# Performance work log

Measured on AMD Instinct MI355X. Metric: run time of the kernel, lower is better.

The kernel has to match this reference:

```python
import math
import jax, jax.numpy as jnp
import numpy as np

K_KDE = 50
K_RIPS = 16
SCALE = 30.0
DESTNUM = 10
THRESHOLD = 1.0  # hardcoded in topograd_loss
N, D = 8192, 64


def _knn(x, k):
    """Brute-force k-NN with squared L2 distances (faiss IndexFlatL2 semantics,
    self included as nearest neighbour). Returns (sq_dists[N,k], idxs[N,k]),
    neighbours sorted by increasing distance."""
    sq = jnp.sum(x * x, axis=1)
    d = sq[:, None] + sq[None, :] - 2.0 * (x @ x.T)  # [N,N]
    neg, idx = jax.lax.top_k(-d, k)
    return -neg, idx


def _cluster(density, rips_idxs, threshold):
    """Union-find re-implementation of the numba `cluster` routine.
    Iterates points from high density (index N-1) to low; each point joins the
    entry of its highest-index upward neighbour; other upward neighbours'
    entries are merged if their persistence is below threshold, and every
    cross-entry comparison emits a persistence pair (entry_idx, ref_idx).
    Returns the raw pers_pairs array (without the [-1,-1] sentinel rows)."""
    n = density.shape[0]
    parent = np.arange(n)
    name = np.arange(n)  # name[root] = entry id (a point index)

    def find(i):
        root = i
        while parent[root] != root:
            root = parent[root]
        while parent[i] != root:  # path compression
            parent[i], i = root, parent[i]
        return root

    pairs = []
    for i in range(n - 2, -1, -1):
        nbr = rips_idxs[i]
        us = nbr[nbr > i]  # upward (denser, already-processed) neighbours
        if us.size == 0:
            continue  # point i forms its own singleton entry
        e_up = name[find(int(us.max()))]
        parent[find(i)] = find(e_up)  # append i to entry e_up
        for j in us:
            ei = name[find(int(j))]
            if ei != e_up:
                pairs.append((ei, i))
                if density[ei] - density[i] < threshold:
                    parent[find(ei)] = find(e_up)  # merge entry ei into e_up
    return np.asarray(pairs, dtype=np.int64).reshape(-1, 2)


def _pd_pairs(pairs, n):
    """For each unique entry id in pairs[:,0], keep (entry_id, max ref idx)."""
    maxref = np.full(n, -1, dtype=np.int64)
    np.maximum.at(maxref, pairs[:, 0], pairs[:, 1])
    uniq = np.unique(pairs[:, 0])
    return np.stack([uniq, maxref[uniq]], axis=1)


def setup_inputs() -> dict:
    key = jax.random.key(0)
    x = jax.random.normal(key, (N, D), dtype=jnp.float32)
    return {"x": x}


def reference(x):
    # --- KNN kernel density estimate (differentiable) ---
    vals, _ = _knn(x, K_KDE)
    res = jnp.sum(jnp.exp(-vals / SCALE), axis=1) / (K_KDE * SCALE)
    dens = res / jnp.max(res)
    # --- sort by ascending density ---
    sorted_idxs = jnp.argsort(dens)
    dens_s = dens[sorted_idxs]
    x_s = x[sorted_idxs]
    # --- delta-Rips graph on sorted points ---
    _, rips_idxs = _knn(x_s, K_RIPS)
    # --- persistence clustering (non-differentiable, host) ---
    pairs = _cluster(np.asarray(dens_s), np.asarray(rips_idxs), THRESHOLD)
    pd = jnp.asarray(_pd_pairs(pairs, x.shape[0]))  # [P,2] int64
    # --- topological loss ---
    oripd = dens_s[pd]  # [P,2] (birth, death) densities
    sidx = jnp.argsort(oripd[:, 0] - oripd[:, 1])  # ascending persistence
    changepairs = pd[sidx[:-DESTNUM]]
    nochangepairs = pd[sidx[-DESTNUM:-1]]
    dest = jax.lax.stop_gradient(oripd[sidx[-1]])  # torch.as_tensor detaches
    pd11 = dens_s[changepairs]
    weakdist = jnp.sum(pd11[:, 0] - pd11[:, 1]) / math.sqrt(2.0)
    strongdist = jnp.sum(jnp.linalg.norm(dens_s[nochangepairs] - dest, axis=1))
    return weakdist + strongdist
```

## Files before the change

### kernel.cpp

```cpp
#include <hip/hip_runtime.h>
#include <stdint.h>

#define NN 8192
#define DD 64

using bf16x8 = __attribute__((ext_vector_type(8))) short;
using f32x4  = __attribute__((ext_vector_type(4))) float;

__device__ __forceinline__ unsigned short f2bf(float f){
  unsigned u = __float_as_uint(f);
  return (unsigned short)((u + 0x7FFFu + ((u >> 16) & 1u)) >> 16);
}

__device__ __forceinline__ unsigned long long shfl64_xor(unsigned long long v, int off){
  return (((unsigned long long)(unsigned)__shfl_xor((int)(v >> 32), off)) << 32)
       | (unsigned long long)(unsigned)__shfl_xor((int)(v & 0xFFFFFFFFu), off);
}

__global__ __launch_bounds__(256) void k_pre(const float* __restrict__ x, float* __restrict__ xT,
                                             float* __restrict__ sq, int do_tr,
                                             uint4* __restrict__ xfrag, int do_frag){
  __shared__ float tile[64*65];
  const int tid = threadIdx.x;
  const int b = blockIdx.x;
  for (int k = 0; k < 4; ++k){
    const int idx4 = tid + k*256;
    const float4 v = ((const float4*)(x + (size_t)b*4096))[idx4];
    const int row = idx4 >> 4, d0 = (idx4 & 15) * 4;
    tile[row*65 + d0 + 0] = v.x;
    tile[row*65 + d0 + 1] = v.y;
    tile[row*65 + d0 + 2] = v.z;
    tile[row*65 + d0 + 3] = v.w;
  }
  __syncthreads();
  if (do_tr){
    const int jj = tid & 15;
    const int dq = tid >> 4;
    for (int k = 0; k < 4; ++k){
      const int d = dq + 16*k;
      float4 o;
      o.x = tile[(jj*4+0)*65 + d];
      o.y = tile[(jj*4+1)*65 + d];
      o.z = tile[(jj*4+2)*65 + d];
      o.w = tile[(jj*4+3)*65 + d];
      ((float4*)xT)[(size_t)d*2048 + b*16 + jj] = o;
    }
  }
  if (do_frag){
    for (int ch = tid; ch < 512; ch += 256){
      const int c  = ch & 15;
      const int q  = (ch >> 4) & 3;
      const int m  = (ch >> 6) & 1;
      const int gl = ch >> 7;
      const float* sp = tile + (gl*16 + c)*65 + m*32 + q*8;
      unsigned short h[8];
#pragma unroll
      for (int i2 = 0; i2 < 8; ++i2) h[i2] = f2bf(sp[i2]);
      uint4 o;
      o.x = (unsigned)h[0] | ((unsigned)h[1] << 16);
      o.y = (unsigned)h[2] | ((unsigned)h[3] << 16);
      o.z = (unsigned)h[4] | ((unsigned)h[5] << 16);
      o.w = (unsigned)h[6] | ((unsigned)h[7] << 16);
      xfrag[(size_t)b*512 + ch] = o;
    }
  }
  if (tid < 64){
    float acc = 0.f;
    const float* rp = tile + tid*65;
    for (int d = 0; d < 64; ++d) acc = fmaf(rp[d], rp[d], acc);
    sq[b*64 + tid] = acc;
  }
}

template<bool XT>
__device__ __forceinline__ void dists_1024(const float* __restrict__ x, const float* __restrict__ xT,
                                           const float* __restrict__ xi, int jbase, int tid,
                                           float acc[8][4]){
#pragma unroll
  for (int r = 0; r < 8; ++r)
#pragma unroll
    for (int q = 0; q < 4; ++q) acc[r][q] = 0.f;
  const int j0 = jbase + tid*4;
  for (int dq = 0; dq < 16; ++dq){
    float4 vj[4];
    if (XT){
#pragma unroll
      for (int s = 0; s < 4; ++s)
        vj[s] = ((const float4*)xT)[(size_t)(dq*4+s)*2048 + (j0 >> 2)];
    } else {
#pragma unroll
      for (int s = 0; s < 4; ++s){
        const int d = dq*4 + s;
        vj[s].x = x[(size_t)(j0+0)*64 + d];
        vj[s].y = x[(size_t)(j0+1)*64 + d];
        vj[s].z = x[(size_t)(j0+2)*64 + d];
        vj[s].w = x[(size_t)(j0+3)*64 + d];
      }
    }
#pragma unroll
    for (int r = 0; r < 8; ++r){
      const float4 wv = ((const float4*)(xi + r*64))[dq];
      acc[r][0] = fmaf(vj[0].x, wv.x, acc[r][0]);
      acc[r][1] = fmaf(vj[0].y, wv.x, acc[r][1]);
      acc[r][2] = fmaf(vj[0].z, wv.x, acc[r][2]);
      acc[r][3] = fmaf(vj[0].w, wv.x, acc[r][3]);
      acc[r][0] = fmaf(vj[1].x, wv.y, acc[r][0]);
      acc[r][1] = fmaf(vj[1].y, wv.y, acc[r][1]);
      acc[r][2] = fmaf(vj[1].z, wv.y, acc[r][2]);
      acc[r][3] = fmaf(vj[1].w, wv.y, acc[r][3]);
      acc[r][0] = fmaf(vj[2].x, wv.z, acc[r][0]);
      acc[r][1] = fmaf(vj[2].y, wv.z, acc[r][1]);
      acc[r][2] = fmaf(vj[2].z, wv.z, acc[r][2]);
      acc[r][3] = fmaf(vj[2].w, wv.z, acc[r][3]);
      acc[r][0] = fmaf(vj[3].x, wv.w, acc[r][0]);
      acc[r][1] = fmaf(vj[3].y, wv.w, acc[r][1]);
      acc[r][2] = fmaf(vj[3].z, wv.w, acc[r][2]);
      acc[r][3] = fmaf(vj[3].w, wv.w, acc[r][3]);
    }
  }
}

template<bool XT>
__global__ __launch_bounds__(256) void k_samp(const float* __restrict__ x, const float* __restrict__ xT,
                                              const float* __restrict__ sq, float* __restrict__ tub){
  __shared__ __align__(16) float xi[8*64];
  __shared__ float sqi_s[8];
  __shared__ __align__(16) float samp[8*1024];
  const int tid = threadIdx.x;
  const int i0 = blockIdx.x * 8;
  for (int t = tid; t < 8*64; t += 256) xi[t] = x[(size_t)i0*64 + t];
  if (tid < 8) sqi_s[tid] = sq[i0+tid];
  __syncthreads();
  float sqir[8];
#pragma unroll
  for (int r = 0; r < 8; ++r) sqir[r] = sqi_s[r];

  const int w0 = (blockIdx.x * 1024) & 8191;
  float acc[8][4];
  dists_1024<XT>(x, xT, xi, w0, tid, acc);
  float sqj[4];
#pragma unroll
  for (int q = 0; q < 4; ++q) sqj[q] = sq[w0 + tid*4 + q];
#pragma unroll
  for (int r = 0; r < 8; ++r)
#pragma unroll
    for (int q = 0; q < 4; ++q)
      samp[r*1024 + tid*4 + q] = (sqir[r] + sqj[q]) - 2.f*acc[r][q];
  __syncthreads();
  const int wv = tid >> 6, lane = tid & 63;
  for (int rr = 0; rr < 2; ++rr){
    const int r = wv + rr*4;
    float v[16];
#pragma unroll
    for (int k2 = 0; k2 < 16; ++k2) v[k2] = samp[r*1024 + lane + 64*k2];
    unsigned lo = 0u, hi = 0x7F800001u;
    while (hi - lo > 1u){
      const unsigned mid = (lo + hi) >> 1;
      const float pf = __uint_as_float(mid);
      int c = 0;
#pragma unroll
      for (int k2 = 0; k2 < 16; ++k2) c += (v[k2] < pf) ? 1 : 0;
#pragma unroll
      for (int off = 32; off; off >>= 1) c += __shfl_xor(c, off);
      if (c >= 32) hi = mid; else lo = mid;
    }
    if (lane == 0) tub[i0 + r] = __uint_as_float(hi);
  }
}

__global__ __launch_bounds__(256) void k_filt(const float* __restrict__ x, const float* __restrict__ sq,
                                              const float* __restrict__ tub,
                                              const uint4* __restrict__ xfrag,
                                              unsigned char* __restrict__ nib){
  const int tid = threadIdx.x;
  const int l   = tid & 63;
  const int w   = tid >> 6;
  const int qh  = l >> 4;
  const int c16 = l & 15;
  const int i0  = blockIdx.x * 8;

  bf16x8 a0, a1;
#pragma unroll
  for (int i2 = 0; i2 < 8; ++i2){ a0[i2] = 0; a1[i2] = 0; }
  if (c16 < 8){
    const float* ap = x + (size_t)(i0 + c16)*64 + qh*8;
#pragma unroll
    for (int i2 = 0; i2 < 8; ++i2){
      a0[i2] = (short)f2bf(ap[i2]);
      a1[i2] = (short)f2bf(ap[i2 + 32]);
    }
  }
  float thr3[4], rs[4];
#pragma unroll
  for (int rg = 0; rg < 4; ++rg){
    int row = qh*4 + rg; row = (row < 8) ? row : 0;
    thr3[rg] = (tub[i0 + row] - sq[i0 + row]) + 0.002f;
    rs[rg]   = 0.017f * sqrtf(sq[i0 + row]);
  }

  const bf16x8* bfp = (const bf16x8*)xfrag + (size_t)w*128 + l;
  const float*  sqp = sq + w*16 + c16;
  unsigned char* nb = nib + (size_t)blockIdx.x*8192 + w*16 + c16;

  bf16x8 A0 = bfp[0],   A1 = bfp[64];     float SA = sqp[0];
  bf16x8 B0 = bfp[512], B1 = bfp[512+64]; float SB = sqp[64];
  for (int it = 0; it < 128; it += 2){
    const int n2 = (it+2 < 128) ? it+2 : 126;
    const int n3 = (it+3 < 128) ? it+3 : 127;
    bf16x8 N0 = bfp[(size_t)n2*512], N1 = bfp[(size_t)n2*512 + 64];
    bf16x8 M0 = bfp[(size_t)n3*512], M1 = bfp[(size_t)n3*512 + 64];
    const float SN = sqp[n2*64], SM = sqp[n3*64];
    {
      f32x4 acc = {0.f, 0.f, 0.f, 0.f};
      acc = __builtin_amdgcn_mfma_f32_16x16x32_bf16(a0, A0, acc, 0, 0, 0);
      acc = __builtin_amdgcn_mfma_f32_16x16x32_bf16(a1, A1, acc, 0, 0, 0);
      const float sr = sqrtf(SA);
      unsigned m4 = 0u;
      m4 |= (fmaf(-rs[0], sr, fmaf(-2.f, acc[0], SA)) < thr3[0]) ? 1u : 0u;
      m4 |= (fmaf(-rs[1], sr, fmaf(-2.f, acc[1], SA)) < thr3[1]) ? 2u : 0u;
      m4 |= (fmaf(-rs[2], sr, fmaf(-2.f, acc[2], SA)) < thr3[2]) ? 4u : 0u;
      m4 |= (fmaf(-rs[3], sr, fmaf(-2.f, acc[3], SA)) < thr3[3]) ? 8u : 0u;
      const unsigned pm = (unsigned)__shfl((int)m4, (l + 16) & 63);
      if (l < 16) nb[it*64] = (unsigned char)(m4 | (pm << 4));
    }
    {
      f32x4 acc = {0.f, 0.f, 0.f, 0.f};
      acc = __builtin_amdgcn_mfma_f32_16x16x32_bf16(a0, B0, acc, 0, 0, 0);
      acc = __builtin_amdgcn_mfma_f32_16x16x32_bf16(a1, B1, acc, 0, 0, 0);
      const float sr = sqrtf(SB);
      unsigned m4 = 0u;
      m4 |= (fmaf(-rs[0], sr, fmaf(-2.f, acc[0], SB)) < thr3[0]) ? 1u : 0u;
      m4 |= (fmaf(-rs[1], sr, fmaf(-2.f, acc[1], SB)) < thr3[1]) ? 2u : 0u;
      m4 |= (fmaf(-rs[2], sr, fmaf(-2.f, acc[2], SB)) < thr3[2]) ? 4u : 0u;
      m4 |= (fmaf(-rs[3], sr, fmaf(-2.f, acc[3], SB)) < thr3[3]) ? 8u : 0u;
      const unsigned pm = (unsigned)__shfl((int)m4, (l + 16) & 63);
      if (l < 16) nb[(it+1)*64] = (unsigned char)(m4 | (pm << 4));
    }
    A0 = N0; A1 = N1; SA = SN;
    B0 = M0; B1 = M1; SB = SM;
  }
}

__global__ __launch_bounds__(256, 4) void k_csort(const float* __restrict__ x, const float* __restrict__ sq,
                                                  const float* __restrict__ tub,
                                                  const unsigned char* __restrict__ nib,
                                                  float* __restrict__ res, unsigned short* __restrict__ nn16){
  __shared__ __align__(16) float xi[4*68];
  __shared__ float sqi_s[4];
  __shared__ float tubs[4];
  __shared__ __align__(16) unsigned long long cand[4*512];
  __shared__ unsigned ccnt[4];
  const int tid  = threadIdx.x;
  const int grp  = blockIdx.x >> 1;
  const int half = blockIdx.x & 1;
  const int i0   = grp*8 + half*4;
  const unsigned rmask = half ? 0xF0F0F0F0u : 0x0F0F0F0Fu;

  for (int t = tid; t < 4*64; t += 256) xi[(t >> 6)*68 + (t & 63)] = x[(size_t)i0*64 + t];
  if (tid < 4){ sqi_s[tid] = sq[i0+tid]; tubs[tid] = tub[i0+tid]; ccnt[tid] = 0u; }
  for (int t = tid; t < 4*512; t += 256) cand[t] = ~0ULL;
  __syncthreads();

  const uint4* nb4 = (const uint4*)(nib + (size_t)grp*8192);
  for (int u = tid; u < 512; u += 256){
    const uint4 v4 = nb4[u];
    unsigned wds[4] = {v4.x & rmask, v4.y & rmask, v4.z & rmask, v4.w & rmask};
#pragma unroll
    for (int ww = 0; ww < 4; ++ww){
      unsigned wvv = wds[ww];
      while (wvv){
        const int bit = __builtin_ctz(wvv);
        wvv &= wvv - 1u;
        const int r = bit & 3;
        const int j = u*16 + ww*4 + (bit >> 3);
        const float* xj = x + (size_t)j*64;
        const float* xr = xi + r*68;
        float acc = 0.f;
#pragma unroll
        for (int d4 = 0; d4 < 16; ++d4){
          const float4 vj4 = ((const float4*)xj)[d4];
          const float4 wi4 = ((const float4*)xr)[d4];
          acc = fmaf(vj4.x, wi4.x, acc);
          acc = fmaf(vj4.y, wi4.y, acc);
          acc = fmaf(vj4.z, wi4.z, acc);
          acc = fmaf(vj4.w, wi4.w, acc);
        }
        const float dist = (sqi_s[r] + sq[j]) - 2.f*acc;
        if (dist < tubs[r]){
          const unsigned pos = atomicAdd(&ccnt[r], 1u);
          if (pos < 512u){
            unsigned u2 = __float_as_uint(dist);
            u2 = ((int)u2 < 0) ? ~u2 : (u2 | 0x80000000u);
            cand[r*512 + pos] = (((unsigned long long)u2) << 13) | (unsigned)j;
          }
        }
      }
    }
  }
  __syncthreads();

  const int w = tid >> 6, lane = tid & 63;
  {
    const int r = w;
    unsigned long long k8[8];
#pragma unroll
    for (int t = 0; t < 8; ++t) k8[t] = cand[r*512 + lane + 64*t];

    const unsigned long long REALMAX = (1ULL << 45) - 1ULL;
    int creal = 0;
#pragma unroll
    for (int t = 0; t < 8; ++t) creal += (int)__popcll(__ballot(k8[t] <= REALMAX));

    unsigned long long K50;
    if (creal >= 50){
      unsigned long long lo = 0ULL, hi = REALMAX;
      while (lo < hi){
        const unsigned long long mid = lo + ((hi - lo) >> 1);
        int c = 0;
#pragma unroll
        for (int t = 0; t < 8; ++t) c += (int)__popcll(__ballot(k8[t] <= mid));
        if (c >= 50) hi = mid; else lo = mid + 1ULL;
      }
      K50 = hi;
    } else {
      K50 = ~0ULL;
    }

    unsigned long long* buf = cand + r*512;
    buf[lane] = ~0ULL;
    int base = 0;
#pragma unroll
    for (int t = 0; t < 8; ++t){
      const bool pr = (k8[t] <= K50) && (k8[t] != ~0ULL);
      const unsigned long long bal = __ballot(pr);
      const int off = base + (int)__popcll(bal & ((1ULL << lane) - 1ULL));
      if (pr && off < 64) buf[off] = k8[t];
      base += (int)__popcll(bal);
    }
    unsigned long long key = buf[lane];

#pragma unroll
    for (int k = 2; k <= 64; k <<= 1){
#pragma unroll
      for (int j = k >> 1; j > 0; j >>= 1){
        const unsigned long long p = shfl64_xor(key, j);
        const bool dirUp = ((lane & k) == 0);
        const bool lower = ((lane & j) == 0);
        const unsigned long long mn = (key < p) ? key : p;
        const unsigned long long mx = (key < p) ? p : key;
        key = (dirUp == lower) ? mn : mx;
      }
    }

    float e = 0.f;
    if (lane < 50){
      unsigned u2 = (unsigned)(key >> 13);
      u2 = (u2 & 0x80000000u) ? (u2 & 0x7FFFFFFFu) : ~u2;
      e = expf(-__uint_as_float(u2) / 30.f);
    }
#pragma unroll
    for (int off = 32; off; off >>= 1) e += __shfl_down(e, off);
    if (lane == 0) res[i0+r] = e / 1500.f;
    if (lane < 16) nn16[(size_t)(i0+r)*16 + lane] = (unsigned short)(key & 8191ULL);
  }
}

template<bool XT>
__global__ __launch_bounds__(256) void k_cand(const float* __restrict__ x, const float* __restrict__ xT,
                                              const float* __restrict__ sq,
                                              float* __restrict__ res, unsigned short* __restrict__ nn16){
  __shared__ float xi[8*64];
  __shared__ float sqi_s[8];
  __shared__ float tubs[8];
  __shared__ __align__(16) unsigned long long cand[8*512];
  __shared__ unsigned ccnt[8];
  float* samp = (float*)cand;
  const int tid = threadIdx.x;
  const int i0 = blockIdx.x * 8;
  for (int t = tid; t < 8*64; t += 256) xi[t] = x[(size_t)i0*64 + t];
  if (tid < 8){ sqi_s[tid] = sq[i0+tid]; ccnt[tid] = 0u; }
  __syncthreads();
  float sqir[8];
#pragma unroll
  for (int r = 0; r < 8; ++r) sqir[r] = sqi_s[r];

  const int w0 = (blockIdx.x * 1024) & 8191;
  {
    float acc[8][4];
    dists_1024<XT>(x, xT, xi, w0, tid, acc);
    float sqj[4];
#pragma unroll
    for (int q = 0; q < 4; ++q) sqj[q] = sq[w0 + tid*4 + q];
#pragma unroll
    for (int r = 0; r < 8; ++r)
#pragma unroll
      for (int q = 0; q < 4; ++q)
        samp[r*1024 + tid*4 + q] = (sqir[r] + sqj[q]) - 2.f*acc[r][q];
  }
  __syncthreads();
  {
    const int wv = tid >> 6, lane = tid & 63;
    for (int rr = 0; rr < 2; ++rr){
      const int r = wv + rr*4;
      float v[16];
#pragma unroll
      for (int k2 = 0; k2 < 16; ++k2) v[k2] = samp[r*1024 + lane + 64*k2];
      unsigned lo = 0u, hi = 0x7F800001u;
      while (hi - lo > 1u){
        const unsigned mid = (lo + hi) >> 1;
        const float pf = __uint_as_float(mid);
        int c = 0;
#pragma unroll
        for (int k2 = 0; k2 < 16; ++k2) c += (v[k2] < pf) ? 1 : 0;
#pragma unroll
        for (int off = 32; off; off >>= 1) c += __shfl_xor(c, off);
        if (c >= 32) hi = mid; else lo = mid;
      }
      if (lane == 0) tubs[r] = __uint_as_float(hi);
    }
  }
  __syncthreads();
  float tubr[8];
#pragma unroll
  for (int r = 0; r < 8; ++r) tubr[r] = tubs[r];
  for (int t = tid; t < 8*512; t += 256) cand[t] = ~0ULL;
  __syncthreads();

  for (int pass = 0; pass < 8; ++pass){
    const int jb = pass*1024;
    float acc[8][4];
    dists_1024<XT>(x, xT, xi, jb, tid, acc);
    const int j0 = jb + tid*4;
    float sqj[4];
#pragma unroll
    for (int q = 0; q < 4; ++q) sqj[q] = sq[j0 + q];
#pragma unroll
    for (int r = 0; r < 8; ++r){
#pragma unroll
      for (int q = 0; q < 4; ++q){
        const float dist = (sqir[r] + sqj[q]) - 2.f*acc[r][q];
        if (dist < tubr[r]){
          const unsigned pos = atomicAdd(&ccnt[r], 1u);
          if (pos < 512u){
            unsigned u = __float_as_uint(dist);
            u = ((int)u < 0) ? ~u : (u | 0x80000000u);
            cand[r*512 + pos] = (((unsigned long long)u) << 13) | (unsigned)(j0 + q);
          }
        }
      }
    }
  }
  __syncthreads();

  for (int k = 2; k <= 512; k <<= 1){
    for (int jj2 = k >> 1; jj2 > 0; jj2 >>= 1){
      const int mm = tid;
      const int i = ((mm & ~(jj2-1)) << 1) | (mm & (jj2-1));
      const int p = i | jj2;
      const bool up2 = ((i & k) == 0);
#pragma unroll
      for (int r = 0; r < 8; ++r){
        unsigned long long a = cand[r*512+i], bb = cand[r*512+p];
        if ((a > bb) == up2){ cand[r*512+i] = bb; cand[r*512+p] = a; }
      }
      __syncthreads();
    }
  }

  const int wv2 = tid >> 6, lane2 = tid & 63;
  for (int rr = 0; rr < 2; ++rr){
    const int r = wv2*2 + rr;
    const unsigned long long kk = cand[r*512 + lane2];
    float e = 0.f;
    if (lane2 < 50){
      unsigned u2 = (unsigned)(kk >> 13);
      u2 = (u2 & 0x80000000u) ? (u2 & 0x7FFFFFFFu) : ~u2;
      e = expf(-__uint_as_float(u2) / 30.f);
    }
#pragma unroll
    for (int off = 32; off; off >>= 1) e += __shfl_down(e, off);
    if (lane2 == 0) res[i0+r] = e / 1500.f;
    if (lane2 < 16) nn16[(size_t)(i0+r)*16 + lane2] = (unsigned short)(kk & 8191ULL);
  }
}

__global__ __launch_bounds__(256) void k_rank(const float* __restrict__ res,
                                              unsigned short* __restrict__ rank,
                                              float* __restrict__ dens_s){
  __shared__ __align__(16) unsigned long long keys[NN];
  __shared__ float red[256];
  __shared__ unsigned short pcnt[256];
  const int tid = threadIdx.x;
  float m = 0.f;
  for (int t = tid; t < NN; t += 256) m = fmaxf(m, res[t]);
  red[tid] = m; __syncthreads();
  for (int o = 128; o; o >>= 1){ if (tid < o) red[tid] = fmaxf(red[tid], red[tid+o]); __syncthreads(); }
  const float mr = red[0];
  __syncthreads();
  for (int t = tid; t < NN; t += 256){
    const float dnv = res[t] / mr;
    keys[t] = (((unsigned long long)__float_as_uint(dnv)) << 13) | (unsigned)t;
  }
  __syncthreads();
  const int i = blockIdx.x*128 + (tid & 127);
  const unsigned long long ki = keys[i];
  const int j0 = (tid >> 7) * (NN/2);
  int c = 0;
#pragma unroll 8
  for (int j = 0; j < NN/2; ++j) c += (keys[j0 + j] < ki) ? 1 : 0;
  pcnt[tid] = (unsigned short)c;
  __syncthreads();
  if (tid < 128){
    const int r = (int)pcnt[tid] + (int)pcnt[tid + 128];
    rank[i] = (unsigned short)r;
    dens_s[r] = __uint_as_float((unsigned)(ki >> 13));
  }
}

__global__ __launch_bounds__(256) void k_ups(const unsigned short* __restrict__ rank,
                                             const unsigned short* __restrict__ nn16,
                                             unsigned short* __restrict__ ups_t){
  __shared__ __align__(16) unsigned short rk[NN];
  const int tid = threadIdx.x;
  for (int t = tid; t < NN/8; t += 256) ((uint4*)rk)[t] = ((const uint4*)rank)[t];
  __syncthreads();
  const int o = blockIdx.x*256 + tid;
  const int p = rk[o];
  const uint4 n0 = ((const uint4*)nn16)[(size_t)o*2];
  const uint4 n1 = ((const uint4*)nn16)[(size_t)o*2 + 1];
  unsigned nw[8] = {n0.x, n0.y, n0.z, n0.w, n1.x, n1.y, n1.z, n1.w};
  unsigned short outv[16];
  int cnt = 0;
  for (int k = 0; k < 16; ++k){
    const unsigned nb = (nw[k >> 1] >> ((k & 1) * 16)) & 0xFFFFu;
    const unsigned r = rk[nb];
    if ((int)r > p){
      int q = cnt++;
      while (q > 0 && outv[q-1] < (unsigned short)r){ outv[q] = outv[q-1]; --q; }
      outv[q] = (unsigned short)r;
    }
  }
  for (int k = cnt; k < 16; ++k) outv[k] = 0;
  unsigned short* dst = ups_t + (size_t)p*16;
  uint4 a, b;
  a.x = (unsigned)outv[0] | ((unsigned)outv[1] << 16);
  a.y = (unsigned)outv[2] | ((unsigned)outv[3] << 16);
  a.z = (unsigned)outv[4] | ((unsigned)outv[5] << 16);
  a.w = (unsigned)outv[6] | ((unsigned)outv[7] << 16);
  b.x = (unsigned)outv[8] | ((unsigned)outv[9] << 16);
  b.y = (unsigned)outv[10] | ((unsigned)outv[11] << 16);
  b.z = (unsigned)outv[12] | ((unsigned)outv[13] << 16);
  b.w = (unsigned)outv[14] | ((unsigned)outv[15] << 16);
  ((uint4*)dst)[0] = a;
  ((uint4*)dst)[1] = b;
}

__device__ __forceinline__ unsigned uf_find2(volatile unsigned short* comp, unsigned x){
  unsigned r = comp[x];
  while (true){
    const unsigned g = comp[r];
    if (g == r) break;
    comp[x] = (unsigned short)g;
    x = r; r = g;
  }
  return r;
}

__global__ __launch_bounds__(1024) void k_msf(const float* __restrict__ dens_s,
                                              unsigned short* __restrict__ ups_t,
                                              unsigned long long* __restrict__ edges,
                                              int edgecap,
                                              float* __restrict__ out){
  __shared__ __align__(16) float dens[NN];
  __shared__ __align__(16) unsigned short P[NN];
  __shared__ __align__(16) unsigned short pkid[NN];
  __shared__ __align__(16) unsigned short death[NN];
  __shared__ __align__(16) unsigned short pkrank[4096];
  __shared__ __align__(16) unsigned short comp[4096];
  __shared__ __align__(16) unsigned short hook[4096];
  __shared__ __align__(16) unsigned bestv[4096];
  __shared__ __align__(16) unsigned long long msf[4096];
  __shared__ unsigned long long sel[10];
  __shared__ unsigned ecnt_s, ecnt2_s, mcnt_s, chg_s, flat_s, dcnt_s;
  unsigned* scan1 = (unsigned*)msf;
  float* red = (float*)msf;
  unsigned* dlist = bestv;

  const int tid = threadIdx.x;
  const int lane = tid & 63;

  for (int t = tid; t < NN/4; t += 1024)
    ((float4*)dens)[t] = ((const float4*)dens_s)[t];
  for (int t = tid; t < NN; t += 1024){
    const unsigned u0 = ups_t[(size_t)t*16];
    P[t] = (u0 == 0u) ? (unsigned short)t : (unsigned short)u0;
    death[t] = 0xFFFFu;
  }
  if (tid == 0){ ecnt_s = 0u; mcnt_s = 0u; dcnt_s = 0u; }
  __syncthreads();

  for (int rd = 0; rd < 13; ++rd){
    for (int pp = 0; pp < 8; ++pp){
      const int p = tid + pp*1024;
      const unsigned v = P[p];
      const unsigned w2 = P[v];
      if (w2 != v) P[p] = (unsigned short)w2;
    }
    __syncthreads();
  }

  {
    const int p0 = tid*8;
    int c = 0;
    for (int k = 0; k < 8; ++k) c += (P[p0+k] == (unsigned short)(p0+k)) ? 1 : 0;
    unsigned v = (unsigned)c;
    for (int s = 1; s < 64; s <<= 1){
      const unsigned o = (unsigned)__shfl_up((int)v, s);
      if (lane >= s) v += o;
    }
    if (lane == 63) scan1[1024 + (tid >> 6)] = v;
    __syncthreads();
    if (tid < 16){
      unsigned wv2 = scan1[1024 + tid];
      for (int s = 1; s < 16; s <<= 1){
        const unsigned o = (unsigned)__shfl_up((int)wv2, s);
        if (tid >= s) wv2 += o;
      }
      scan1[1040 + tid] = wv2;
    }
    __syncthreads();
    const unsigned woff = (tid >= 64) ? scan1[1040 + (tid >> 6) - 1] : 0u;
    const unsigned incl = v + woff;
    if (tid == 1023) scan1[1023] = incl;
    int base = (int)incl - c;
    for (int k = 0; k < 8; ++k){
      const int p = p0 + k;
      if (P[p] == (unsigned short)p){
        pkid[p] = (unsigned short)base;
        if (base < 4096) pkrank[base] = (unsigned short)p;
        ++base;
      }
    }
  }
  __syncthreads();
  int Npk = (int)scan1[1023];
  if (Npk > 4096) Npk = 4096;
  __syncthreads();

  for (int pp = 0; pp < 8; ++pp){
    const int p = tid + pp*1024;
    const uint4 a4 = ((const uint4*)ups_t)[(size_t)p*2];
    const uint4 b4 = ((const uint4*)ups_t)[(size_t)p*2 + 1];
    unsigned uu[8] = {a4.x, a4.y, a4.z, a4.w, b4.x, b4.y, b4.z, b4.w};
    unsigned edv[15];
    int nd = 0;
    const unsigned u0 = uu[0] & 0xFFFFu;
    if (u0 != 0u){
      const unsigned m0 = P[u0];
      const unsigned m0id = pkid[m0];
      for (int k = 1; k < 16; ++k){
        const unsigned uk = (uu[k >> 1] >> ((k & 1) * 16)) & 0xFFFFu;
        if (uk == 0u) break;
        const unsigned v = P[uk];
        if (v == m0) continue;
        const unsigned vid = pkid[v];
        bool dup = false;
        for (int j = 0; j < nd; ++j) dup = dup || ((edv[j] >> 16) == vid);
        if (dup) continue;
        edv[nd++] = (vid << 16) | m0id;
      }
    }
    unsigned off = (unsigned)nd;
    for (int s = 1; s < 64; s <<= 1){
      const unsigned o = (unsigned)__shfl_up((int)off, s);
      if (lane >= s) off += o;
    }
    const unsigned tot = (unsigned)__shfl((int)off, 63);
    unsigned wb = 0u;
    if (lane == 0 && tot) wb = atomicAdd(&ecnt_s, tot);
    wb = (unsigned)__shfl((int)wb, 0);
    const unsigned mybase = wb + off - (unsigned)nd;
    for (int k = 0; k < nd; ++k){
      const unsigned pos = mybase + (unsigned)k;
      if ((int)pos < edgecap)
        edges[pos] = (((unsigned long long)(unsigned)p) << 32) | (unsigned long long)edv[k];
    }
  }
  __syncthreads();
  int Ecur = ((int)ecnt_s < edgecap) ? (int)ecnt_s : edgecap;

  unsigned long long* eb_in  = edges;
  unsigned long long* eb_out = (unsigned long long*)ups_t;
  for (int t = tid; t < Npk; t += 1024) comp[t] = (unsigned short)t;
  __syncthreads();
  for (int round = 0; round < 16 && Ecur > 0; ++round){
    for (int t = tid; t < Npk; t += 1024){ bestv[t] = 0u; hook[t] = 0xFFFFu; }
    if (tid == 0){ chg_s = 0u; ecnt2_s = 0u; }
    __syncthreads();
    for (int base = 0; base < Ecur; base += 1024){
      const int e = base + tid;
      bool keep = false;
      unsigned long long ed = 0ULL;
      if (e < Ecur){
        ed = eb_in[e];
        const unsigned a = (unsigned)(ed >> 16) & 0xFFFFu;
        const unsigned b = (unsigned)ed & 0xFFFFu;
        const unsigned ra = comp[a], rb = comp[b];
        if (ra != rb){
          keep = true;
          const unsigned key = ((((unsigned)(ed >> 32)) + 1u) << 18) | (unsigned)e;
          atomicMax(&bestv[ra], key);
          atomicMax(&bestv[rb], key);
        }
      }
      const unsigned long long bal = __ballot(keep);
      const unsigned cnt = (unsigned)__popcll(bal);
      const unsigned pfx = (unsigned)__popcll(bal & ((1ULL << lane) - 1ULL));
      unsigned wb = 0u;
      if (lane == 0 && cnt) wb = atomicAdd(&ecnt2_s, cnt);
      wb = (unsigned)__shfl((int)wb, 0);
      if (keep && (wb + pfx) < 32768u) eb_out[wb + pfx] = ed;
    }
    __syncthreads();
    for (int t = tid; t < Npk; t += 1024){
      if (comp[t] == (unsigned short)t && bestv[t] != 0u){
        const unsigned long long ed = eb_in[bestv[t] & 0x3FFFFu];
        const unsigned a = (unsigned)(ed >> 16) & 0xFFFFu;
        const unsigned b = (unsigned)ed & 0xFFFFu;
        const unsigned ra = comp[a], rb = comp[b];
        hook[t] = (unsigned short)((ra == (unsigned)t) ? rb : ra);
      }
    }
    __syncthreads();
    for (int t = tid; t < Npk; t += 1024){
      const unsigned o = hook[t];
      if (o != 0xFFFFu && !(hook[o] == (unsigned short)t && (unsigned)t < o)){
        comp[t] = (unsigned short)o;
        chg_s = 1u;
        const unsigned long long ed = eb_in[bestv[t] & 0x3FFFFu];
        const unsigned pos = atomicAdd(&mcnt_s, 1u);
        if (pos < 4096u) msf[pos] = (((ed >> 32) + 1ULL) << 32) | (ed & 0xFFFFFFFFULL);
      }
    }
    __syncthreads();
    for (;;){
      if (tid == 0) flat_s = 0u;
      __syncthreads();
      for (int t = tid; t < Npk; t += 1024){
        const unsigned c = comp[t];
        const unsigned cc = comp[c];
        if (cc != c){ comp[t] = (unsigned short)cc; flat_s = 1u; }
      }
      __syncthreads();
      if (flat_s == 0u) break;
    }
    const int En = ((int)ecnt2_s < 32768) ? (int)ecnt2_s : 32767;
    const unsigned ch = chg_s;
    __syncthreads();
    Ecur = En;
    { unsigned long long* t2 = eb_in; eb_in = eb_out; eb_out = t2; }
    if (ch == 0u) break;
  }

  const int M = ((int)mcnt_s < 4096) ? (int)mcnt_s : 4095;
  int W = 64; while (W < M) W <<= 1;
  for (int t = M + tid; t < W; t += 1024) msf[t] = 0ULL;
  for (int t = tid; t < Npk; t += 1024) comp[t] = (unsigned short)t;
  __syncthreads();
  for (int k = 2; k <= W; k <<= 1){
    for (int j = k >> 1; j > 0; j >>= 1){
      for (int m2 = tid; m2 < W/2; m2 += 1024){
        const int i = ((m2 & ~(j-1)) << 1) | (m2 & (j-1));
        const int p = i | j;
        const bool up = ((i & k) == 0);
        const unsigned long long a = msf[i], b = msf[p];
        if ((a < b) == up){ msf[i] = b; msf[p] = a; }
      }
      __syncthreads();
    }
  }

  {
    const int nb = (M + 63) >> 6;
    if (tid < 64){
      for (int bch = 0; bch < nb; ++bch){
        const int ei = bch*64 + lane;
        unsigned ra = 0xFFFFu, rb = 0xFFFFu, wgt = 0u;
        if (ei < M){
          const unsigned long long e = msf[ei];
          const unsigned a = ((unsigned)e >> 16) & 0xFFFFu;
          const unsigned b = (unsigned)e & 0xFFFFu;
          wgt = (unsigned)(e >> 32) - 1u;
          ra = uf_find2(comp, a);
          rb = uf_find2(comp, b);
        }
        unsigned kra = 0xFFFFu, krb = 0xFFFFu;
        for (int i = 0; i < 64; ++i){
          const unsigned rai = (unsigned)__builtin_amdgcn_readlane((int)ra, i);
          const unsigned rbi = (unsigned)__builtin_amdgcn_readlane((int)rb, i);
          if (rai == 0xFFFFu || rai == rbi) continue;
          if (lane == i){ kra = rai; krb = rbi; }
          ra = (ra == rai) ? rbi : ra;
          rb = (rb == rai) ? rbi : rb;
        }
        if (kra != 0xFFFFu){
          death[pkrank[kra]] = (unsigned short)wgt;
          comp[kra] = (unsigned short)krb;
        }
      }
    }
    __syncthreads();
  }

  float s = 0.f;
  for (int e = tid; e < NN; e += 1024){
    const int dr = death[e];
    if (dr != 0xFFFF) s += dens[e] - dens[dr];
  }
  red[tid] = s; __syncthreads();
  for (int o = 512; o; o >>= 1){ if (tid < o) red[tid] += red[tid+o]; __syncthreads(); }
  const float S = red[0];

  for (int e8 = 0; e8 < 8; ++e8){
    const int e = tid + e8*1024;
    const int dr = death[e];
    const bool have = (dr != 0xFFFF);
    const unsigned long long bal = __ballot(have);
    const unsigned cnt = (unsigned)__popcll(bal);
    const unsigned pfx = (unsigned)__popcll(bal & ((1ULL << lane) - 1ULL));
    unsigned wb = 0u;
    if (lane == 0 && cnt) wb = atomicAdd(&dcnt_s, cnt);
    wb = (unsigned)__shfl((int)wb, 0);
    if (have && (wb + pfx) < 4096u) dlist[wb + pfx] = ((unsigned)e << 13) | (unsigned)dr;
  }
  __syncthreads();
  const int Dm = ((int)dcnt_s < 4096) ? (int)dcnt_s : 4096;

  if (tid < 64){
    unsigned long long last = ~0ULL;
    for (int t10 = 0; t10 < 10; ++t10){
      unsigned long long km = 0ULL;
      for (int i = lane; i < Dm; i += 64){
        const unsigned pk = dlist[i];
        const unsigned e = pk >> 13, dr = pk & 8191u;
        const float pers = dens[e] - dens[dr];
        const unsigned long long k = (((unsigned long long)__float_as_uint(pers)) << 13) | e;
        if (k < last && k > km) km = k;
      }
      for (int off = 32; off; off >>= 1){
        const unsigned long long o = shfl64_xor(km, off);
        km = (o > km) ? o : km;
      }
      if (lane == 0) sel[t10] = km;
      last = km;
    }
  }
  __syncthreads();
  if (tid == 0){
    float top = 0.f;
    for (int t10 = 0; t10 < 10; ++t10)
      if (sel[t10]) top += __uint_as_float((unsigned)(sel[t10] >> 13));
    float strong = 0.f, dest0 = 0.f, dest1 = 0.f;
    if (sel[0]){
      const unsigned e0 = (unsigned)(sel[0] & 8191ULL);
      dest0 = dens[e0]; dest1 = dens[death[e0]];
    }
    for (int t10 = 1; t10 < 10; ++t10){
      if (!sel[t10]) continue;
      const unsigned e = (unsigned)(sel[t10] & 8191ULL);
      const float a = dens[e] - dest0;
      const float b = dens[death[e]] - dest1;
      strong += sqrtf(a*a + b*b);
    }
    out[0] = (S - top) / 1.41421356237309515f + strong;
  }
}

extern "C" void kernel_launch(void* const* d_in, const int* in_sizes, int n_in,
                              void* d_out, int out_size, void* d_ws, size_t ws_size,
                              hipStream_t stream){
  const float* x = (const float*)d_in[0];
  char* w = (char*)d_ws;
  float*          sq     = (float*)(w + 0);
  float*          res    = (float*)(w + 32768);
  float*          dens_s = (float*)(w + 65536);
  unsigned short* rank   = (unsigned short*)(w + 98304);
  unsigned short* nn16   = (unsigned short*)(w + 114688);
  unsigned short* ups_t  = (unsigned short*)(w + 376832);
  float*          xT     = (float*)(w + 655360);
  uint4*          xfrag  = (uint4*)(w + 2752512);
  float*          tub    = (float*)(w + 3801088);
  unsigned char*  nib    = (unsigned char*)(w + 3833856);
  const int use_xt  = (ws_size >= (size_t)2752512) ? 1 : 0;
  const int use_mf2 = (ws_size >= (size_t)(3833856 + 8*1024*1024)) ? 1 : 0;
  unsigned long long* edges = use_xt ? (unsigned long long*)(w + 655360)
                                     : (unsigned long long*)(w + 114688);
  const int edgecap = use_xt ? 262143 : 32767;

  k_pre<<<128, 256, 0, stream>>>(x, xT, sq, use_xt, xfrag, use_mf2);
  if (use_mf2){
    k_samp<true><<<1024, 256, 0, stream>>>(x, xT, sq, tub);
    k_filt<<<1024, 256, 0, stream>>>(x, sq, tub, xfrag, nib);
    k_csort<<<2048, 256, 0, stream>>>(x, sq, tub, nib, res, nn16);
  } else if (use_xt){
    k_cand<true ><<<1024, 256, 0, stream>>>(x, xT, sq, res, nn16);
  } else {
    k_cand<false><<<1024, 256, 0, stream>>>(x, xT, sq, res, nn16);
  }
  k_rank<<<64, 256, 0, stream>>>(res, rank, dens_s);
  k_ups <<<32, 256, 0, stream>>>(rank, nn16, ups_t);
  k_msf <<<1, 1024, 0, stream>>>(dens_s, ups_t, edges, edgecap, (float*)d_out);
}
```

Baseline: 571.8 us.

## Compact candidates into shared pool and verify with balanced wave-wide dot products

k_csort now handles 8 query rows per block instead of 4, so each block reads its nib filter group once and the grid is halved. Surviving candidate bits are compacted into a shared pool using a wave prefix sum. The exact distance checks then run over that pool with two lanes per candidate, each loading half of the 64-wide row, instead of one thread looping serially over an uneven number of set bits. This targets load imbalance and divergence in the candidate-refinement loop, at the cost of more shared memory per block (lower occupancy), and a pool overflow path that keeps the old serial computation.

After: 537.4 us. 6.0% less time.

```diff
diff --git a/kernel.cpp b/kernel.cpp
--- a/kernel.cpp
+++ b/kernel.cpp
@@ -3,6 +3,7 @@
 
 #define NN 8192
 #define DD 64
+#define POOLCAP 6144
 
 using bf16x8 = __attribute__((ext_vector_type(8))) short;
 using f32x4  = __attribute__((ext_vector_type(4))) float;
@@ -245,63 +246,139 @@
                                                   const float* __restrict__ tub,
                                                   const unsigned char* __restrict__ nib,
                                                   float* __restrict__ res, unsigned short* __restrict__ nn16){
-  __shared__ __align__(16) float xi[4*68];
-  __shared__ float sqi_s[4];
-  __shared__ float tubs[4];
-  __shared__ __align__(16) unsigned long long cand[4*512];
-  __shared__ unsigned ccnt[4];
+  __shared__ __align__(16) float xi[8*68];
+  __shared__ float sqi_s[8];
+  __shared__ float tubs[8];
+  __shared__ __align__(16) unsigned long long cand[8*512];
+  __shared__ unsigned ccnt[8];
+  __shared__ __align__(16) unsigned short pool[POOLCAP];
+  __shared__ unsigned pcnt_s;
   const int tid  = threadIdx.x;
-  const int grp  = blockIdx.x >> 1;
-  const int half = blockIdx.x & 1;
-  const int i0   = grp*8 + half*4;
-  const unsigned rmask = half ? 0xF0F0F0F0u : 0x0F0F0F0Fu;
-
-  for (int t = tid; t < 4*64; t += 256) xi[(t >> 6)*68 + (t & 63)] = x[(size_t)i0*64 + t];
-  if (tid < 4){ sqi_s[tid] = sq[i0+tid]; tubs[tid] = tub[i0+tid]; ccnt[tid] = 0u; }
-  for (int t = tid; t < 4*512; t += 256) cand[t] = ~0ULL;
-  __syncthreads();
-
-  const uint4* nb4 = (const uint4*)(nib + (size_t)grp*8192);
-  for (int u = tid; u < 512; u += 256){
-    const uint4 v4 = nb4[u];
-    unsigned wds[4] = {v4.x & rmask, v4.y & rmask, v4.z & rmask, v4.w & rmask};
-#pragma unroll
-    for (int ww = 0; ww < 4; ++ww){
+  const int lane = tid & 63;
+  const int w    = tid >> 6;
+  const int grp  = blockIdx.x;
+  const int i0   = grp*8;
+
+  for (int t = tid; t < 8*64; t += 256) xi[(t >> 6)*68 + (t & 63)] = x[(size_t)i0*64 + t];
+  if (tid < 8){ sqi_s[tid] = sq[i0+tid]; tubs[tid] = tub[i0+tid]; ccnt[tid] = 0u; }
+  if (tid == 0) pcnt_s = 0u;
+  for (int t = tid; t < 8*512; t += 256) cand[t] = ~0ULL;
+  __syncthreads();
+
+  {
+    const uint4* nb4 = (const uint4*)(nib + (size_t)grp*8192);
+    const uint4 vA = nb4[tid];
+    const uint4 vB = nb4[tid + 256];
+    unsigned wds[8] = {vA.x, vA.y, vA.z, vA.w, vB.x, vB.y, vB.z, vB.w};
+    int cnt = 0;
+#pragma unroll
+    for (int ww = 0; ww < 8; ++ww) cnt += __popc(wds[ww]);
+    int incl = cnt;
+    for (int s = 1; s < 64; s <<= 1){
+      const int o = __shfl_up(incl, s);
+      if (lane >= s) incl += o;
+    }
+    const unsigned tot = (unsigned)__shfl(incl, 63);
+    unsigned wb = 0u;
+    if (lane == 0 && tot) wb = atomicAdd(&pcnt_s, tot);
+    wb = (unsigned)__shfl((int)wb, 0);
+    int myoff = (int)wb + incl - cnt;
+#pragma unroll
+    for (int ww = 0; ww < 8; ++ww){
+      const int u = (ww < 4) ? tid : tid + 256;
+      const int colbase = u*16 + (ww & 3)*4;
       unsigned wvv = wds[ww];
       while (wvv){
         const int bit = __builtin_ctz(wvv);
         wvv &= wvv - 1u;
-        const int r = bit & 3;
-        const int j = u*16 + ww*4 + (bit >> 3);
-        const float* xj = x + (size_t)j*64;
-        const float* xr = xi + r*68;
-        float acc = 0.f;
-#pragma unroll
-        for (int d4 = 0; d4 < 16; ++d4){
-          const float4 vj4 = ((const float4*)xj)[d4];
-          const float4 wi4 = ((const float4*)xr)[d4];
-          acc = fmaf(vj4.x, wi4.x, acc);
-          acc = fmaf(vj4.y, wi4.y, acc);
-          acc = fmaf(vj4.z, wi4.z, acc);
-          acc = fmaf(vj4.w, wi4.w, acc);
-        }
-        const float dist = (sqi_s[r] + sq[j]) - 2.f*acc;
-        if (dist < tubs[r]){
-          const unsigned pos = atomicAdd(&ccnt[r], 1u);
-          if (pos < 512u){
-            unsigned u2 = __float_as_uint(dist);
-            u2 = ((int)u2 < 0) ? ~u2 : (u2 | 0x80000000u);
-            cand[r*512 + pos] = (((unsigned long long)u2) << 13) | (unsigned)j;
+        const int r = bit & 7;
+        const int j = colbase + (bit >> 3);
+        if (myoff < POOLCAP){
+          pool[myoff] = (unsigned short)((r << 13) | j);
+        } else {
+          const float* xj = x + (size_t)j*64;
+          const float* xr = xi + r*68;
+          float acc = 0.f;
+#pragma unroll
+          for (int d4 = 0; d4 < 16; ++d4){
+            const float4 a = ((const float4*)xj)[d4];
+            const float4 b = ((const float4*)xr)[d4];
+            acc = fmaf(a.x, b.x, acc);
+            acc = fmaf(a.y, b.y, acc);
+            acc = fmaf(a.z, b.z, acc);
+            acc = fmaf(a.w, b.w, acc);
+          }
+          const float dist = (sqi_s[r] + sq[j]) - 2.f*acc;
+          if (dist < tubs[r]){
+            const unsigned pos = atomicAdd(&ccnt[r], 1u);
+            if (pos < 512u){
+              unsigned u2 = __float_as_uint(dist);
+              u2 = ((int)u2 < 0) ? ~u2 : (u2 | 0x80000000u);
+              cand[r*512 + pos] = (((unsigned long long)u2) << 13) | (unsigned)j;
+            }
           }
         }
-      }
-    }
-  }
-  __syncthreads();
-
-  const int w = tid >> 6, lane = tid & 63;
+        ++myoff;
+      }
+    }
+  }
+  __syncthreads();
+  const int P = ((int)pcnt_s < POOLCAP) ? (int)pcnt_s : POOLCAP;
+
   {
-    const int r = w;
+    const int c  = lane >> 1;
+    const int k2 = lane & 1;
+    for (int base = w*32; base < P; base += 128){
+      const int ci = base + c;
+      const bool valid = ci < P;
+      const unsigned e = valid ? (unsigned)pool[ci] : 0u;
+      const int j = (int)(e & 8191u);
+      const int r = (int)(e >> 13);
+      const float4* xj = (const float4*)(x + (size_t)j*64 + k2*32);
+      const float4* xr = (const float4*)(xi + r*68 + k2*32);
+      float4 vv[8];
+#pragma unroll
+      for (int d4 = 0; d4 < 8; ++d4) vv[d4] = xj[d4];
+      float acc = 0.f;
+      if (k2 == 0){
+#pragma unroll
+        for (int d4 = 0; d4 < 8; ++d4){
+          const float4 a = vv[d4], b = xr[d4];
+          acc = fmaf(a.x, b.x, acc);
+          acc = fmaf(a.y, b.y, acc);
+          acc = fmaf(a.z, b.z, acc);
+          acc = fmaf(a.w, b.w, acc);
+        }
+      }
+      const float passed = __shfl_xor(acc, 1);
+      if (k2 == 1){
+        acc = passed;
+#pragma unroll
+        for (int d4 = 0; d4 < 8; ++d4){
+          const float4 a = vv[d4], b = xr[d4];
+          acc = fmaf(a.x, b.x, acc);
+          acc = fmaf(a.y, b.y, acc);
+          acc = fmaf(a.z, b.z, acc);
+          acc = fmaf(a.w, b.w, acc);
+        }
+        if (valid){
+          const float dist = (sqi_s[r] + sq[j]) - 2.f*acc;
+          if (dist < tubs[r]){
+            const unsigned pos = atomicAdd(&ccnt[r], 1u);
+            if (pos < 512u){
+              unsigned u2 = __float_as_uint(dist);
+              u2 = ((int)u2 < 0) ? ~u2 : (u2 | 0x80000000u);
+              cand[r*512 + pos] = (((unsigned long long)u2) << 13) | (unsigned)j;
+            }
+          }
+        }
+      }
+    }
+  }
+  __syncthreads();
+
+  for (int rr = 0; rr < 2; ++rr){
+    const int r = w + rr*4;
     unsigned long long k8[8];
 #pragma unroll
     for (int t = 0; t < 8; ++t) k8[t] = cand[r*512 + lane + 64*t];
@@ -901,7 +978,7 @@
   if (use_mf2){
     k_samp<true><<<1024, 256, 0, stream>>>(x, xT, sq, tub);
     k_filt<<<1024, 256, 0, stream>>>(x, sq, tub, xfrag, nib);
-    k_csort<<<2048, 256, 0, stream>>>(x, sq, tub, nib, res, nn16);
+    k_csort<<<1024, 256, 0, stream>>>(x, sq, tub, nib, res, nn16);
   } else if (use_xt){
     k_cand<true ><<<1024, 256, 0, stream>>>(x, xT, sq, res, nn16);
   } else {
```
